# Optimization experiments

Measured on AMD Instinct MI355X. Metric: run time of the kernel, lower is better.

## Reference

```python
import jax, jax.numpy as jnp
import numpy as np

WS = 7          # window size
SHIFT = WS // 2 # shift for odd blocks
NH = 8          # num heads
EPS = 1e-5


def _rel_pos_index(ws):
    coords = np.stack(np.meshgrid(np.arange(ws), np.arange(ws), indexing='ij'))  # (2, ws, ws)
    cf = coords.reshape(2, -1)                                  # (2, N)
    rc = (cf[:, :, None] - cf[:, None, :]).transpose(1, 2, 0)   # (N, N, 2)
    rc[..., 0] += ws - 1
    rc[..., 1] += ws - 1
    rc[..., 0] *= 2 * ws - 1
    return rc.sum(-1)  # (N, N) int


def _attn_mask(Hp, Wp, ws, shift):
    # (nW, N, N) additive mask with 0 / -100, as in the torch code
    img = np.zeros((Hp, Wp), dtype=np.float32)
    cnt = 0
    slices = (slice(0, -ws), slice(-ws, -shift), slice(-shift, None))
    for h in slices:
        for w in slices:
            img[h, w] = cnt
            cnt += 1
    mw = img.reshape(Hp // ws, ws, Wp // ws, ws).transpose(0, 2, 1, 3).reshape(-1, ws * ws)
    am = mw[:, None, :] - mw[:, :, None]
    return np.where(am != 0, -100.0, 0.0).astype(np.float32)


def _layernorm(x, w, b):
    m = x.mean(-1, keepdims=True)
    v = ((x - m) ** 2).mean(-1, keepdims=True)
    return (x - m) * jax.lax.rsqrt(v + EPS) * w + b


def _window_partition(x, ws):
    B, H, W, C = x.shape
    x = x.reshape(B, H // ws, ws, W // ws, ws, C).transpose(0, 1, 3, 2, 4, 5)
    return x.reshape(-1, ws * ws, C)


def _window_reverse(w, ws, H, W):
    B = w.shape[0] // (H // ws * W // ws)
    x = w.reshape(B, H // ws, W // ws, ws, ws, -1).transpose(0, 1, 3, 2, 4, 5)
    return x.reshape(B, H, W, -1)


def _window_msa(xw, qkv_w, qkv_b, proj_w, proj_b, rpb, rel_idx, mask):
    Bw, N, C = xw.shape
    hd = C // NH
    qkv = (xw @ qkv_w.T + qkv_b).reshape(Bw, N, 3, NH, hd).transpose(2, 0, 3, 1, 4)
    q, k, v = qkv[0] * (hd ** -0.5), qkv[1], qkv[2]
    attn = jnp.einsum('bhnd,bhmd->bhnm', q, k)                      # (Bw, NH, N, N)
    bias = rpb[rel_idx.reshape(-1)].reshape(N, N, NH).transpose(2, 0, 1)
    attn = attn + bias[None]
    if mask is not None:
        nW = mask.shape[0]
        attn = attn.reshape(Bw // nW, nW, NH, N, N) + mask[None, :, None]
        attn = attn.reshape(Bw, NH, N, N)
    attn = jax.nn.softmax(attn, axis=-1)
    out = jnp.einsum('bhnm,bhmd->bhnd', attn, v).transpose(0, 2, 1, 3).reshape(Bw, N, C)
    return out @ proj_w.T + proj_b


def _forward(x, ln1_w, ln1_b, qkv_w, qkv_b, proj_w, proj_b, rpb,
             ln2_w, ln2_b, mlp_w1, mlp_b1, mlp_w2, mlp_b2, H, W):
    B, L, C = x.shape
    rel_idx = _rel_pos_index(WS)
    pad_r = (WS - W % WS) % WS
    pad_b = (WS - H % WS) % WS
    Hp, Wp = H + pad_b, W + pad_r
    depth = ln1_w.shape[0]
    for i in range(depth):
        shift = 0 if i % 2 == 0 else SHIFT
        shortcut = x
        h = _layernorm(x, ln1_w[i], ln1_b[i]).reshape(B, H, W, C)
        if pad_r > 0 or pad_b > 0:
            h = jnp.pad(h, ((0, 0), (0, pad_b), (0, pad_r), (0, 0)))
        if shift > 0:
            h = jnp.roll(h, (-shift, -shift), axis=(1, 2))
            mask = jnp.asarray(_attn_mask(Hp, Wp, WS, shift))
        else:
            mask = None
        hw = _window_partition(h, WS)
        hw = _window_msa(hw, qkv_w[i], qkv_b[i], proj_w[i], proj_b[i], rpb[i], rel_idx, mask)
        h = _window_reverse(hw.reshape(-1, WS, WS, C), WS, Hp, Wp)
        if shift > 0:
            h = jnp.roll(h, (shift, shift), axis=(1, 2))
        if pad_r > 0 or pad_b > 0:
            h = h[:, :H, :W, :]
        x = shortcut + h.reshape(B, H * W, C)
        m = _layernorm(x, ln2_w[i], ln2_b[i])
        m = jax.nn.gelu(m @ mlp_w1[i].T + mlp_b1[i], approximate=False)
        x = x + (m @ mlp_w2[i].T + mlp_b2[i])
    return x


def setup_inputs() -> dict:
    key = jax.random.key(0)
    ks = jax.random.split(key, 8)
    B, H, W, C, D = 8, 112, 112, 256, 2
    hid = 4 * C
    return {
        'x': jax.random.normal(ks[0], (B, H * W, C), jnp.float32),
        'ln1_w': jnp.ones((D, C), jnp.float32),
        'ln1_b': jnp.zeros((D, C), jnp.float32),
        'qkv_w': jax.random.normal(ks[1], (D, 3 * C, C), jnp.float32) * 0.02,
        'qkv_b': jnp.zeros((D, 3 * C), jnp.float32),
        'proj_w': jax.random.normal(ks[2], (D, C, C), jnp.float32) * 0.02,
        'proj_b': jnp.zeros((D, C), jnp.float32),
        'rpb': jax.random.normal(ks[3], (D, (2 * WS - 1) ** 2, NH), jnp.float32) * 0.02,
        'ln2_w': jnp.ones((D, C), jnp.float32),
        'ln2_b': jnp.zeros((D, C), jnp.float32),
        'mlp_w1': jax.random.normal(ks[4], (D, hid, C), jnp.float32) * 0.02,
        'mlp_b1': jnp.zeros((D, hid), jnp.float32),
        'mlp_w2': jax.random.normal(ks[5], (D, C, hid), jnp.float32) * 0.02,
        'mlp_b2': jnp.zeros((D, C), jnp.float32),
        'H': H,
        'W': W,
    }


def reference(x, ln1_w, ln1_b, qkv_w, qkv_b, proj_w, proj_b, rpb,
              ln2_w, ln2_b, mlp_w1, mlp_b1, mlp_w2, mlp_b2, H, W):
    return _forward(x, ln1_w, ln1_b, qkv_w, qkv_b, proj_w, proj_b, rpb,
                    ln2_w, ln2_b, mlp_w1, mlp_b1, mlp_w2, mlp_b2, H, W)
```

## Files before the change

### kernel.cpp

```cpp
#include <hip/hip_runtime.h>

typedef unsigned short u16;
typedef unsigned int u32;
typedef __attribute__((ext_vector_type(8))) short bf16x8;
typedef __attribute__((ext_vector_type(4))) float f32x4;
typedef __attribute__((ext_vector_type(16))) float f32x16;
typedef __attribute__((ext_vector_type(8))) unsigned short u16x8;
typedef const __attribute__((address_space(1))) void gvoid;
typedef __attribute__((address_space(3))) void svoid;

#define T_TOK 100352
#define CDIM 256
#define ATTN_SCALE 0.17677669529663687f

__device__ __forceinline__ u16 f2bf(float f) {
    u32 u = __float_as_uint(f);
    u32 r = (u + 0x7fffu + ((u >> 16) & 1u)) >> 16;
    return (u16)r;
}
__device__ __forceinline__ float bf2f(u16 h) {
    return __uint_as_float(((u32)h) << 16);
}
__device__ __forceinline__ u32 cvtpk(float lo, float hi) {
    u32 r;
    asm("v_cvt_pk_bf16_f32 %0, %1, %2" : "=v"(r) : "v"(lo), "v"(hi));
    return r;
}
__device__ __forceinline__ float gelu_f(float x) {
    float z = 0.7978845608028654f * (x + 0.044715f * x * x * x);
    float e = __expf(2.0f * z);
    float th = 1.0f - 2.0f * __builtin_amdgcn_rcpf(e + 1.0f);
    return 0.5f * x * (1.0f + th);
}
__device__ __forceinline__ int div7(int q) { return (q * 37) >> 8; }
__device__ __forceinline__ int reg3(int r) { return r < 105 ? 0 : (r < 109 ? 1 : 2); }

__global__ void cvt_kernel(const float* __restrict__ in, u16* __restrict__ out, int n) {
    int i = blockIdx.x * 256 + threadIdx.x;
    if (i < n) out[i] = f2bf(in[i]);
}

__global__ __launch_bounds__(256) void ln_kernel(
    const float* __restrict__ X, const float* __restrict__ w,
    const float* __restrict__ b, u16* __restrict__ Y)
{
    int wid = threadIdx.x >> 6, l = threadIdx.x & 63;
    int t = blockIdx.x * 4 + wid;
    const float4 x4 = ((const float4*)(X + (size_t)t * CDIM))[l];
    float s  = x4.x + x4.y + x4.z + x4.w;
    float s2 = x4.x*x4.x + x4.y*x4.y + x4.z*x4.z + x4.w*x4.w;
    #pragma unroll
    for (int o = 32; o; o >>= 1) { s += __shfl_xor(s, o); s2 += __shfl_xor(s2, o); }
    float mean = s * (1.0f/256.0f);
    float var  = s2 * (1.0f/256.0f) - mean*mean;
    float rstd = rsqrtf(var + 1e-5f);
    float4 w4 = ((const float4*)w)[l];
    float4 b4 = ((const float4*)b)[l];
    ushort4 o4;
    o4.x = f2bf((x4.x - mean)*rstd*w4.x + b4.x);
    o4.y = f2bf((x4.y - mean)*rstd*w4.y + b4.y);
    o4.z = f2bf((x4.z - mean)*rstd*w4.z + b4.z);
    o4.w = f2bf((x4.w - mean)*rstd*w4.w + b4.w);
    ((ushort4*)(Y + (size_t)t * CDIM))[l] = o4;
}

template<int EPI>
__global__ __launch_bounds__(256) void gemm_kernel(
    const u16* __restrict__ A, const u16* __restrict__ Bw,
    const float* __restrict__ bias, void* __restrict__ outp,
    const float* __restrict__ res, int N, int K, int nTn)
{
    __shared__ __align__(16) char lds_raw[69632];
    u16 (*lds)[2][128 * 64] = (u16(*)[2][128 * 64])lds_raw;
    const int tid = threadIdx.x;
    const int l = tid & 63;
    const int w = tid >> 6;
    const int wr = w >> 1, wc = w & 1;

    const int nBlocks = gridDim.x;
    const int cpx = nBlocks >> 3;
    const int lin = (blockIdx.x & 7) * cpx + (blockIdx.x >> 3);
    const int nT = lin % nTn;
    const int mT = lin / nTn;

    f32x4 acc[4][4];
    #pragma unroll
    for (int m = 0; m < 4; ++m)
        #pragma unroll
        for (int n = 0; n < 4; ++n) acc[m][n] = (f32x4){0.f,0.f,0.f,0.f};

    const int sr = tid >> 3;
    const int sg = tid & 7;

    #define STAGE(buf, kt)                                                              \
        {                                                                               \
            _Pragma("unroll")                                                           \
            for (int c = 0; c < 4; ++c) {                                               \
                int r = c*32 + sr;                                                      \
                int gsrc = sg ^ (r & 7);                                                \
                const u16* ga = A  + (size_t)(mT*128 + r) * K + (kt) + gsrc*8;          \
                const u16* gb = Bw + (size_t)(nT*128 + r) * K + (kt) + gsrc*8;          \
                u16* la = &lds[buf][0][(c*256 + w*64) * 8];                              \
                u16* lb = &lds[buf][1][(c*256 + w*64) * 8];                              \
                __builtin_amdgcn_global_load_lds((gvoid*)ga, (svoid*)la, 16, 0, 0);     \
                __builtin_amdgcn_global_load_lds((gvoid*)gb, (svoid*)lb, 16, 0, 0);     \
            }                                                                           \
        }

    const int nSteps = K >> 6;
    int cur = 0;

    STAGE(0, 0);
    asm volatile("s_waitcnt vmcnt(0)" ::: "memory");
    __builtin_amdgcn_s_barrier();
    asm volatile("" ::: "memory");

    const int lr = l & 15, gq = l >> 4;
    for (int t = 0; t < nSteps; ++t) {
        bf16x8 a[2][4], b[2][4];
        #pragma unroll
        for (int kk = 0; kk < 2; ++kk) {
            #pragma unroll
            for (int m = 0; m < 4; ++m) {
                int r = wr*64 + m*16 + lr;
                int g = kk*4 + gq;
                a[kk][m] = *(const bf16x8*)&lds[cur][0][r*64 + (g ^ (r & 7))*8];
            }
            #pragma unroll
            for (int n = 0; n < 4; ++n) {
                int r = wc*64 + n*16 + lr;
                int g = kk*4 + gq;
                b[kk][n] = *(const bf16x8*)&lds[cur][1][r*64 + (g ^ (r & 7))*8];
            }
        }
        if (t + 1 < nSteps) STAGE(cur ^ 1, (t + 1) * 64);

        __builtin_amdgcn_s_setprio(1);
        #pragma unroll
        for (int kk = 0; kk < 2; ++kk)
            #pragma unroll
            for (int m = 0; m < 4; ++m)
                #pragma unroll
                for (int n = 0; n < 4; ++n)
                    acc[m][n] = __builtin_amdgcn_mfma_f32_16x16x32_bf16(a[kk][m], b[kk][n], acc[m][n], 0, 0, 0);
        __builtin_amdgcn_s_setprio(0);

        asm volatile("s_waitcnt vmcnt(0)" ::: "memory");
        __builtin_amdgcn_s_barrier();
        asm volatile("" ::: "memory");
        cur ^= 1;
    }
    #undef STAGE

    if (EPI == 2) {
        float* epf = (float*)lds_raw + w * (64 * 68);
        #pragma unroll
        for (int m = 0; m < 4; ++m)
            #pragma unroll
            for (int n = 0; n < 4; ++n) {
                float bb = bias[nT*128 + wc*64 + n*16 + lr];
                #pragma unroll
                for (int j = 0; j < 4; ++j)
                    epf[(m*16 + gq*4 + j)*68 + n*16 + lr] = acc[m][n][j] + bb;
            }
        const int rr4 = l >> 4, cc4 = (l & 15) * 4;
        float* outf = (float*)outp;
        #pragma unroll
        for (int p = 0; p < 16; ++p) {
            float4 vv = *(const float4*)&epf[(p*4 + rr4)*68 + cc4];
            size_t grow = (size_t)(mT*128 + wr*64 + p*4 + rr4);
            size_t gcol = (size_t)(nT*128 + wc*64 + cc4);
            float4 rv = *(const float4*)(res + grow*N + gcol);
            float4 ov; ov.x = vv.x + rv.x; ov.y = vv.y + rv.y;
            ov.z = vv.z + rv.z; ov.w = vv.w + rv.w;
            *(float4*)(outf + grow*N + gcol) = ov;
        }
    } else {
        float* epf = (float*)lds_raw + w * (64 * 68);
        #pragma unroll
        for (int m = 0; m < 4; ++m)
            #pragma unroll
            for (int n = 0; n < 4; ++n) {
                float bb = bias[nT*128 + wc*64 + n*16 + lr];
                #pragma unroll
                for (int j = 0; j < 4; ++j) {
                    float v = acc[m][n][j] + bb;
                    if (EPI == 1) v = gelu_f(v);
                    epf[(m*16 + gq*4 + j)*68 + n*16 + lr] = v;
                }
            }
        const int rr8 = l >> 3, cc8 = (l & 7) * 8;
        u16* outw = (u16*)outp;
        #pragma unroll
        for (int p = 0; p < 8; ++p) {
            float4 v0 = *(const float4*)&epf[(p*8 + rr8)*68 + cc8];
            float4 v1 = *(const float4*)&epf[(p*8 + rr8)*68 + cc8 + 4];
            union { u32 u[4]; u16x8 v; } pk;
            pk.u[0] = cvtpk(v0.x, v0.y); pk.u[1] = cvtpk(v0.z, v0.w);
            pk.u[2] = cvtpk(v1.x, v1.y); pk.u[3] = cvtpk(v1.z, v1.w);
            size_t grow = (size_t)(mT*128 + wr*64 + p*8 + rr8);
            size_t gcol = (size_t)(nT*128 + wc*64 + cc8);
            *(u16x8*)(outw + grow*N + gcol) = pk.v;
        }
    }
}

__global__ __launch_bounds__(256, 2) void mlp_kernel(
    const u16* __restrict__ Y, const u16* __restrict__ W1,
    const float* __restrict__ B1, const u16* __restrict__ W2,
    const float* __restrict__ B2, const float* __restrict__ res,
    float* __restrict__ xout)
{
    __shared__ __align__(16) char lds_raw[69632];

    const int tid = threadIdx.x;
    const int l = tid & 63;
    const int w = tid >> 6;
    const int lo = l & 31;
    const int hi = l >> 5;
    const int row0 = blockIdx.x * 128 + w * 32;

    bf16x8 yf[16];
    #pragma unroll
    for (int kt = 0; kt < 16; ++kt)
        yf[kt] = *(const bf16x8*)(Y + (size_t)(row0 + lo) * 256 + kt*16 + hi*8);

    float b2v[8];
    #pragma unroll
    for (int ot = 0; ot < 8; ++ot) b2v[ot] = B2[ot*32 + lo];

    ((float4*)(lds_raw + 65536))[tid] = ((const float4*)B1)[tid];

    f32x16 acc[8];
    #pragma unroll
    for (int ot = 0; ot < 8; ++ot) {
        f32x16 z;
        #pragma unroll
        for (int i = 0; i < 16; ++i) z[i] = 0.f;
        acc[ot] = z;
    }

    const int w1r = tid >> 5;
    const int w1s = tid & 31;
    const int w2r = tid >> 2;
    const int w2g = (tid & 3) ^ ((tid >> 2) & 3);

    #define MSTG(buf, ch)                                                                  \
        {                                                                                  \
            _Pragma("unroll")                                                              \
            for (int c = 0; c < 4; ++c) {                                                  \
                int r1 = c*8 + w1r;                                                        \
                const u16* g1 = W1 + (size_t)((ch)*32 + r1)*256 + (w1s ^ r1)*8;            \
                u16* d1 = (u16*)(lds_raw + (buf)*32768 + (c*256 + w*64)*16);               \
                __builtin_amdgcn_global_load_lds((gvoid*)g1, (svoid*)d1, 16, 0, 0);        \
                const u16* g2 = W2 + (size_t)(c*64 + w2r)*1024 + (ch)*32 + w2g*8;          \
                u16* d2 = (u16*)(lds_raw + (buf)*32768 + 16384 + (c*256 + w*64)*16);       \
                __builtin_amdgcn_global_load_lds((gvoid*)g2, (svoid*)d2, 16, 0, 0);        \
            }                                                                              \
        }

    MSTG(0, 0);
    __syncthreads();

    #pragma unroll 1
    for (int ch = 0; ch < 32; ++ch) {
        const int cur = ch & 1;
        const char* w1b = lds_raw + cur*32768;
        const char* w2b = w1b + 16384;

        f32x16 ht;
        #pragma unroll
        for (int i = 0; i < 16; ++i) ht[i] = 0.f;
        #pragma unroll
        for (int kt = 0; kt < 16; ++kt) {
            int slot = (2*kt + hi) ^ lo;
            bf16x8 w1f = *(const bf16x8*)(w1b + lo*512 + slot*16);
            ht = __builtin_amdgcn_mfma_f32_32x32x16_bf16(w1f, yf[kt], ht, 0, 0, 0);
        }

        if (ch + 1 < 32) MSTG(cur ^ 1, ch + 1);

        const float* b1l = (const float*)(lds_raw + 65536) + ch*32;
        #pragma unroll
        for (int i = 0; i < 16; ++i) {
            int r = (i & 3) + 8*(i >> 2) + 4*hi;
            ht[i] = gelu_f(ht[i] + b1l[r]);
        }

        u32 pk[8];
        #pragma unroll
        for (int j = 0; j < 8; ++j) pk[j] = cvtpk(ht[2*j], ht[2*j+1]);
        bf16x8 pa[2];
        #pragma unroll
        for (int s2 = 0; s2 < 2; ++s2) {
            u32 a0 = pk[s2*4 + 0], a1 = pk[s2*4 + 1];
            u32 a2 = pk[s2*4 + 2], a3 = pk[s2*4 + 3];
            asm volatile("v_permlane32_swap_b32 %0, %1" : "+v"(a0), "+v"(a2));
            asm volatile("v_permlane32_swap_b32 %0, %1" : "+v"(a1), "+v"(a3));
            union { u32 u[4]; bf16x8 v; } pf;
            pf.u[0] = a0; pf.u[1] = a1; pf.u[2] = a2; pf.u[3] = a3;
            pa[s2] = pf.v;
        }

        __builtin_amdgcn_s_setprio(1);
        #pragma unroll
        for (int ot = 0; ot < 8; ++ot) {
            #pragma unroll
            for (int ks = 0; ks < 2; ++ks) {
                int r = ot*32 + lo;
                int slot = (2*ks + hi) ^ (r & 3);
                bf16x8 w2f = *(const bf16x8*)(w2b + r*64 + slot*16);
                acc[ot] = __builtin_amdgcn_mfma_f32_32x32x16_bf16(pa[ks], w2f, acc[ot], 0, 0, 0);
            }
        }
        __builtin_amdgcn_s_setprio(0);

        asm volatile("s_waitcnt vmcnt(0)" ::: "memory");
        __builtin_amdgcn_s_barrier();
        asm volatile("" ::: "memory");
    }
    #undef MSTG

    float* scr = (float*)(lds_raw + w * 16640);
    #pragma unroll 1
    for (int half = 0; half < 2; ++half) {
        #pragma unroll
        for (int ot4 = 0; ot4 < 4; ++ot4) {
            int ot = half*4 + ot4;
            #pragma unroll
            for (int i = 0; i < 16; ++i) {
                int r = (i & 3) + 8*(i >> 2) + 4*hi;
                scr[r*130 + ot4*32 + lo] = acc[ot][i] + b2v[ot];
            }
        }
        asm volatile("s_waitcnt lgkmcnt(0)" ::: "memory");
        __builtin_amdgcn_sched_barrier(0);
        const int rr = l >> 5, cc = (l & 31) * 4;
        #pragma unroll
        for (int p = 0; p < 16; ++p) {
            float4 vv = *(const float4*)&scr[(p*2 + rr)*130 + cc];
            size_t off = (size_t)(row0 + p*2 + rr) * 256 + half*128 + cc;
            float4 rv = *(const float4*)(res + off);
            float4 ov; ov.x = vv.x + rv.x; ov.y = vv.y + rv.y;
            ov.z = vv.z + rv.z; ov.w = vv.w + rv.w;
            *(float4*)(xout + off) = ov;
        }
        asm volatile("s_waitcnt lgkmcnt(0)" ::: "memory");
        __builtin_amdgcn_sched_barrier(0);
    }
}

__global__ __launch_bounds__(256) void attn_kernel(
    const u16* __restrict__ qkv, const float* __restrict__ rpb,
    u16* __restrict__ outb, int shift)
{
    __shared__ u16 Vt[8][2048];
    __shared__ float biasl[8 * 176];
    __shared__ int tok[64];

    const int t = threadIdx.x;
    const int w = t >> 6;
    const int l = t & 63;
    const int lo = l & 31;
    const int hi = l >> 5;
    const int win = blockIdx.x;
    const int wj = win & 15, wi = (win >> 4) & 15, bb = win >> 8;

    if (t < 64) {
        int qq = t > 48 ? 48 : t;
        int i = div7(qq), j = qq - i*7;
        int rr = wi*7 + i + shift; if (rr >= 112) rr -= 112;
        int cc = wj*7 + j + shift; if (cc >= 112) cc -= 112;
        tok[t] = bb*12544 + rr*112 + cc;
    }
    for (int i2 = t; i2 < 1352; i2 += 256)
        biasl[(i2 & 7)*176 + (i2 >> 3)] = rpb[i2];
    __syncthreads();

    int iqv[2], jqv[2], regq[2];
    #pragma unroll
    for (int nt = 0; nt < 2; ++nt) {
        int q = nt*32 + lo; int qb = q > 48 ? 48 : q;
        int iq = div7(qb), jq = qb - iq*7;
        iqv[nt] = iq; jqv[nt] = jq;
        regq[nt] = 0;
        if (shift > 0) regq[nt] = reg3(wi*7 + iq)*3 + reg3(wj*7 + jq);
    }

    #pragma unroll 1
    for (int hh = 0; hh < 2; ++hh) {
        const int h = 2*w + hh;

        {
            u16x8 vreg[4];
            if (l < 49) {
                const u16x8* vs = (const u16x8*)(qkv + (size_t)tok[l]*768 + 512 + h*32);
                #pragma unroll
                for (int c4 = 0; c4 < 4; ++c4) vreg[c4] = vs[c4];
            } else {
                #pragma unroll
                for (int c4 = 0; c4 < 4; ++c4) vreg[c4] = (u16x8){0,0,0,0,0,0,0,0};
            }
            u16* vt = &Vt[h][0];
            #pragma unroll
            for (int c4 = 0; c4 < 4; ++c4)
                #pragma unroll
                for (int e = 0; e < 8; ++e)
                    vt[(c4*8 + e)*64 + (l ^ (e << 3))] = vreg[c4][e];
        }

        bf16x8 kf[2][2], qf[2][2];
        #pragma unroll
        for (int mt = 0; mt < 2; ++mt)
            #pragma unroll
            for (int td = 0; td < 2; ++td)
                kf[mt][td] = *(const bf16x8*)(qkv + (size_t)tok[mt*32 + lo]*768 + 256 + h*32 + td*16 + hi*8);
        #pragma unroll
        for (int nt = 0; nt < 2; ++nt)
            #pragma unroll
            for (int td = 0; td < 2; ++td)
                qf[nt][td] = *(const bf16x8*)(qkv + (size_t)tok[nt*32 + lo]*768 + h*32 + td*16 + hi*8);

        f32x16 s[2][2];
        #pragma unroll
        for (int mt = 0; mt < 2; ++mt)
            #pragma unroll
            for (int nt = 0; nt < 2; ++nt) {
                f32x16 z;
                #pragma unroll
                for (int i = 0; i < 16; ++i) z[i] = 0.f;
                s[mt][nt] = z;
            }
        #pragma unroll
        for (int td = 0; td < 2; ++td)
            #pragma unroll
            for (int mt = 0; mt < 2; ++mt)
                #pragma unroll
                for (int nt = 0; nt < 2; ++nt)
                    s[mt][nt] = __builtin_amdgcn_mfma_f32_32x32x16_bf16(kf[mt][td], qf[nt][td], s[mt][nt], 0, 0, 0);

        asm volatile("s_waitcnt lgkmcnt(0)" ::: "memory");
        __builtin_amdgcn_sched_barrier(0);

        const float* bh = biasl + h*176;
        #pragma unroll
        for (int mt = 0; mt < 2; ++mt) {
            #pragma unroll
            for (int i = 0; i < 16; ++i) {
                int r = (i & 3) + 8*(i >> 2) + 4*hi;
                int k = mt*32 + r;
                bool valid = k < 49;
                int kb = valid ? k : 48;
                int ik = div7(kb), jk = kb - ik*7;
                int regk = 0;
                if (shift > 0) regk = reg3(wi*7 + ik)*3 + reg3(wj*7 + jk);
                #pragma unroll
                for (int nt = 0; nt < 2; ++nt) {
                    float v = s[mt][nt][i] * ATTN_SCALE
                            + bh[(iqv[nt] - ik + 6)*13 + (jqv[nt] - jk + 6)];
                    if (shift > 0 && regq[nt] != regk) v -= 100.0f;
                    if (!valid) v = -1e30f;
                    s[mt][nt][i] = v;
                }
            }
        }

        #pragma unroll
        for (int nt = 0; nt < 2; ++nt) {
            float mx = -1e30f;
            #pragma unroll
            for (int i = 0; i < 16; ++i) mx = fmaxf(mx, fmaxf(s[0][nt][i], s[1][nt][i]));
            mx = fmaxf(mx, __shfl_xor(mx, 32));
            float sum = 0.f;
            #pragma unroll
            for (int mt = 0; mt < 2; ++mt)
                #pragma unroll
                for (int i = 0; i < 16; ++i) {
                    float e = __expf(s[mt][nt][i] - mx);
                    s[mt][nt][i] = e;
                    sum += e;
                }
            sum += __shfl_xor(sum, 32);
            float inv = __builtin_amdgcn_rcpf(sum);

            u32 pk[2][8];
            #pragma unroll
            for (int mt = 0; mt < 2; ++mt)
                #pragma unroll
                for (int j = 0; j < 8; ++j)
                    pk[mt][j] = (u32)f2bf(s[mt][nt][2*j] * inv)
                              | ((u32)f2bf(s[mt][nt][2*j + 1] * inv) << 16);

            f32x16 o;
            #pragma unroll
            for (int i = 0; i < 16; ++i) o[i] = 0.f;
            #pragma unroll
            for (int kt = 0; kt < 4; ++kt) {
                const int mt = kt >> 1;
                const int base = (kt & 1) * 4;
                u32 a0 = pk[mt][base + 0], a1 = pk[mt][base + 1];
                u32 a2 = pk[mt][base + 2], a3 = pk[mt][base + 3];
                asm volatile("v_permlane32_swap_b32 %0, %1" : "+v"(a0), "+v"(a2));
                asm volatile("v_permlane32_swap_b32 %0, %1" : "+v"(a1), "+v"(a3));
                union { u32 u[4]; bf16x8 v; } pf;
                pf.u[0] = a0; pf.u[1] = a1; pf.u[2] = a2; pf.u[3] = a3;
                bf16x8 vb = *(const bf16x8*)(&Vt[h][lo*64 + ((kt*16 + hi*8) ^ ((lo & 7) << 3))]);
                o = __builtin_amdgcn_mfma_f32_32x32x16_bf16(pf.v, vb, o, 0, 0, 0);
            }

            #pragma unroll
            for (int i = 0; i < 16; ++i) {
                int q = nt*32 + (i & 3) + 8*(i >> 2) + 4*hi;
                if (q < 49)
                    outb[(size_t)tok[q]*256 + h*32 + lo] = f2bf(o[i]);
            }
        }
    }
}

extern "C" void kernel_launch(void* const* d_in, const int* in_sizes, int n_in,
                              void* d_out, int out_size, void* d_ws, size_t ws_size,
                              hipStream_t stream) {
    const float* x_in   = (const float*)d_in[0];
    const float* ln1_w  = (const float*)d_in[1];
    const float* ln1_b  = (const float*)d_in[2];
    const float* qkv_w  = (const float*)d_in[3];
    const float* qkv_b  = (const float*)d_in[4];
    const float* proj_w = (const float*)d_in[5];
    const float* proj_b = (const float*)d_in[6];
    const float* rpb    = (const float*)d_in[7];
    const float* ln2_w  = (const float*)d_in[8];
    const float* ln2_b  = (const float*)d_in[9];
    const float* mlp_w1 = (const float*)d_in[10];
    const float* mlp_b1 = (const float*)d_in[11];
    const float* mlp_w2 = (const float*)d_in[12];
    const float* mlp_b2 = (const float*)d_in[13];
    float* xout = (float*)d_out;

    char* p = (char*)d_ws;
    u16* wq = (u16*)p;  p += (size_t)2*768*256*2;
    u16* wp = (u16*)p;  p += (size_t)2*256*256*2;
    u16* w1 = (u16*)p;  p += (size_t)2*1024*256*2;
    u16* w2 = (u16*)p;  p += (size_t)2*256*1024*2;
    u16* buf_y   = (u16*)p; p += (size_t)T_TOK*256*2;
    u16* buf_big = (u16*)p;

    {
        int n;
        n = 2*768*256;  cvt_kernel<<<(n+255)/256, 256, 0, stream>>>(qkv_w,  wq, n);
        n = 2*256*256;  cvt_kernel<<<(n+255)/256, 256, 0, stream>>>(proj_w, wp, n);
        n = 2*1024*256; cvt_kernel<<<(n+255)/256, 256, 0, stream>>>(mlp_w1, w1, n);
        n = 2*256*1024; cvt_kernel<<<(n+255)/256, 256, 0, stream>>>(mlp_w2, w2, n);
    }

    for (int i = 0; i < 2; ++i) {
        const int shift = (i == 0) ? 0 : 3;
        const float* xcur = (i == 0) ? x_in : xout;

        ln_kernel<<<T_TOK/4, 256, 0, stream>>>(xcur, ln1_w + i*256, ln1_b + i*256, buf_y);
        gemm_kernel<0><<<784*6, 256, 0, stream>>>(
            buf_y, wq + (size_t)i*768*256, qkv_b + i*768, buf_big, nullptr, 768, 256, 6);
        attn_kernel<<<2048, 256, 0, stream>>>(buf_big, rpb + i*169*8, buf_y, shift);
        gemm_kernel<2><<<784*2, 256, 0, stream>>>(
            buf_y, wp + (size_t)i*256*256, proj_b + i*256, xout, xcur, 256, 256, 2);
        ln_kernel<<<T_TOK/4, 256, 0, stream>>>(xout, ln2_w + i*256, ln2_b + i*256, buf_y);
        mlp_kernel<<<784, 256, 0, stream>>>(
            buf_y, w1 + (size_t)i*1024*256, mlp_b1 + i*1024,
            w2 + (size_t)i*256*1024, mlp_b2 + i*256, xout, xout);
    }
}
```

Baseline: 959.9 us.

## Pre-tile MLP weights into chunk-contiguous layout and split first GEMM accumulators

MLP weights W1 and W2 are converted into a per-chunk, fragment-ordered bf16 layout by new conversion kernels. Each chunk's global-to-LDS copy is then one contiguous, coalesced read, and the LDS fragment reads no longer need XOR swizzle arithmetic. The next-chunk prefetch is issued before the first GEMM instead of after it, giving more overlap. The first GEMM is split into two independent accumulator chains, summed before GELU, to shorten the MFMA dependency chain. This costs extra registers and changes the LDS bank access pattern, which may now produce conflicts.

```diff
diff --git a/kernel.cpp b/kernel.cpp
--- a/kernel.cpp
+++ b/kernel.cpp
@@ -38,6 +38,19 @@
 __global__ void cvt_kernel(const float* __restrict__ in, u16* __restrict__ out, int n) {
     int i = blockIdx.x * 256 + threadIdx.x;
     if (i < n) out[i] = f2bf(in[i]);
+}
+
+__global__ void cvt_w1_kernel(const float* __restrict__ in, u16* __restrict__ out) {
+    int idx = blockIdx.x * 256 + threadIdx.x;
+    int e = idx & 7, r = (idx >> 3) & 31, g = (idx >> 8) & 31;
+    int ch = (idx >> 13) & 31, L = idx >> 18;
+    out[idx] = f2bf(in[(size_t)L*262144 + (ch*32 + r)*256 + g*8 + e]);
+}
+__global__ void cvt_w2_kernel(const float* __restrict__ in, u16* __restrict__ out) {
+    int idx = blockIdx.x * 256 + threadIdx.x;
+    int e = idx & 7, r = (idx >> 3) & 255, g = (idx >> 11) & 3;
+    int ch = (idx >> 13) & 31, L = idx >> 18;
+    out[idx] = f2bf(in[(size_t)L*262144 + r*1024 + ch*32 + g*8 + e]);
 }
 
 __global__ __launch_bounds__(256) void ln_kernel(
@@ -206,8 +219,8 @@
 }
 
 __global__ __launch_bounds__(256, 2) void mlp_kernel(
-    const u16* __restrict__ Y, const u16* __restrict__ W1,
-    const float* __restrict__ B1, const u16* __restrict__ W2,
+    const u16* __restrict__ Y, const u16* __restrict__ W1t,
+    const float* __restrict__ B1, const u16* __restrict__ W2t,
     const float* __restrict__ B2, const float* __restrict__ res,
     float* __restrict__ xout)
 {
@@ -240,27 +253,23 @@
         acc[ot] = z;
     }
 
-    const int w1r = tid >> 5;
-    const int w1s = tid & 31;
-    const int w2r = tid >> 2;
-    const int w2g = (tid & 3) ^ ((tid >> 2) & 3);
-
     #define MSTG(buf, ch)                                                                  \
         {                                                                                  \
             _Pragma("unroll")                                                              \
             for (int c = 0; c < 4; ++c) {                                                  \
-                int r1 = c*8 + w1r;                                                        \
-                const u16* g1 = W1 + (size_t)((ch)*32 + r1)*256 + (w1s ^ r1)*8;            \
+                const u16* g1 = W1t + (size_t)(ch)*8192 + (c*256 + tid)*8;                 \
                 u16* d1 = (u16*)(lds_raw + (buf)*32768 + (c*256 + w*64)*16);               \
                 __builtin_amdgcn_global_load_lds((gvoid*)g1, (svoid*)d1, 16, 0, 0);        \
-                const u16* g2 = W2 + (size_t)(c*64 + w2r)*1024 + (ch)*32 + w2g*8;          \
+                const u16* g2 = W2t + (size_t)(ch)*8192 + (c*256 + tid)*8;                 \
                 u16* d2 = (u16*)(lds_raw + (buf)*32768 + 16384 + (c*256 + w*64)*16);       \
                 __builtin_amdgcn_global_load_lds((gvoid*)g2, (svoid*)d2, 16, 0, 0);        \
             }                                                                              \
         }
 
     MSTG(0, 0);
-    __syncthreads();
+    asm volatile("s_waitcnt vmcnt(0)" ::: "memory");
+    __builtin_amdgcn_s_barrier();
+    asm volatile("" ::: "memory");
 
     #pragma unroll 1
     for (int ch = 0; ch < 32; ++ch) {
@@ -268,23 +277,25 @@
         const char* w1b = lds_raw + cur*32768;
         const char* w2b = w1b + 16384;
 
+        if (ch + 1 < 32) MSTG(cur ^ 1, ch + 1);
+
+        f32x16 ht0, ht1;
+        #pragma unroll
+        for (int i = 0; i < 16; ++i) { ht0[i] = 0.f; ht1[i] = 0.f; }
+        #pragma unroll
+        for (int kt = 0; kt < 16; kt += 2) {
+            bf16x8 w1f0 = *(const bf16x8*)(w1b + (2*kt + hi)*512 + lo*16);
+            bf16x8 w1f1 = *(const bf16x8*)(w1b + (2*kt + 2 + hi)*512 + lo*16);
+            ht0 = __builtin_amdgcn_mfma_f32_32x32x16_bf16(w1f0, yf[kt], ht0, 0, 0, 0);
+            ht1 = __builtin_amdgcn_mfma_f32_32x32x16_bf16(w1f1, yf[kt+1], ht1, 0, 0, 0);
+        }
+
+        const float* b1l = (const float*)(lds_raw + 65536) + ch*32;
         f32x16 ht;
-        #pragma unroll
-        for (int i = 0; i < 16; ++i) ht[i] = 0.f;
-        #pragma unroll
-        for (int kt = 0; kt < 16; ++kt) {
-            int slot = (2*kt + hi) ^ lo;
-            bf16x8 w1f = *(const bf16x8*)(w1b + lo*512 + slot*16);
-            ht = __builtin_amdgcn_mfma_f32_32x32x16_bf16(w1f, yf[kt], ht, 0, 0, 0);
-        }
-
-        if (ch + 1 < 32) MSTG(cur ^ 1, ch + 1);
-
-        const float* b1l = (const float*)(lds_raw + 65536) + ch*32;
         #pragma unroll
         for (int i = 0; i < 16; ++i) {
             int r = (i & 3) + 8*(i >> 2) + 4*hi;
-            ht[i] = gelu_f(ht[i] + b1l[r]);
+            ht[i] = gelu_f(ht0[i] + ht1[i] + b1l[r]);
         }
 
         u32 pk[8];
@@ -307,9 +318,7 @@
         for (int ot = 0; ot < 8; ++ot) {
             #pragma unroll
             for (int ks = 0; ks < 2; ++ks) {
-                int r = ot*32 + lo;
-                int slot = (2*ks + hi) ^ (r & 3);
-                bf16x8 w2f = *(const bf16x8*)(w2b + r*64 + slot*16);
+                bf16x8 w2f = *(const bf16x8*)(w2b + (2*ks + hi)*4096 + (ot*32 + lo)*16);
                 acc[ot] = __builtin_amdgcn_mfma_f32_32x32x16_bf16(pa[ks], w2f, acc[ot], 0, 0, 0);
             }
         }
@@ -540,8 +549,8 @@
     char* p = (char*)d_ws;
     u16* wq = (u16*)p;  p += (size_t)2*768*256*2;
     u16* wp = (u16*)p;  p += (size_t)2*256*256*2;
-    u16* w1 = (u16*)p;  p += (size_t)2*1024*256*2;
-    u16* w2 = (u16*)p;  p += (size_t)2*256*1024*2;
+    u16* w1t = (u16*)p; p += (size_t)2*1024*256*2;
+    u16* w2t = (u16*)p; p += (size_t)2*256*1024*2;
     u16* buf_y   = (u16*)p; p += (size_t)T_TOK*256*2;
     u16* buf_big = (u16*)p;
 
@@ -549,8 +558,8 @@
         int n;
         n = 2*768*256;  cvt_kernel<<<(n+255)/256, 256, 0, stream>>>(qkv_w,  wq, n);
         n = 2*256*256;  cvt_kernel<<<(n+255)/256, 256, 0, stream>>>(proj_w, wp, n);
-        n = 2*1024*256; cvt_kernel<<<(n+255)/256, 256, 0, stream>>>(mlp_w1, w1, n);
-        n = 2*256*1024; cvt_kernel<<<(n+255)/256, 256, 0, stream>>>(mlp_w2, w2, n);
+        cvt_w1_kernel<<<2048, 256, 0, stream>>>(mlp_w1, w1t);
+        cvt_w2_kernel<<<2048, 256, 0, stream>>>(mlp_w2, w2t);
     }
 
     for (int i = 0; i < 2; ++i) {
@@ -565,7 +574,7 @@
             buf_y, wp + (size_t)i*256*256, proj_b + i*256, xout, xcur, 256, 256, 2);
         ln_kernel<<<T_TOK/4, 256, 0, stream>>>(xout, ln2_w + i*256, ln2_b + i*256, buf_y);
         mlp_kernel<<<784, 256, 0, stream>>>(
-            buf_y, w1 + (size_t)i*1024*256, mlp_b1 + i*1024,
-            w2 + (size_t)i*256*1024, mlp_b2 + i*256, xout, xout);
-    }
-}
+            buf_y, w1t + (size_t)i*262144, mlp_b1 + i*1024,
+            w2t + (size_t)i*262144, mlp_b2 + i*256, xout, xout);
+    }
+}
```

Measured after the change: 961.7 us. About the same (+0.2%).
